# Kernel tuning notes

Hardware: AMD Instinct MI355X
Metric: run time of the kernel (lower is better)

The kernel has to match this reference:

```python
import jax, jax.numpy as jnp
import numpy as np

N_NODES = 50000
N_EDGES = 800000
NDIM_IN = 64
EDIMS = 64
NDIM_OUT = 128


def setup_inputs() -> dict:
    key = jax.random.key(0)
    k = jax.random.split(key, 8)
    nfeats = jax.random.normal(k[0], (N_NODES, NDIM_IN), dtype=jnp.float32)
    efeats = jax.random.normal(k[1], (N_EDGES, EDIMS), dtype=jnp.float32)
    # Linear weights stored as [in, out]; scaled for stable activations.
    W_msg = jax.random.normal(k[2], (NDIM_IN + EDIMS, NDIM_OUT), dtype=jnp.float32) * 0.05
    b_msg = jax.random.normal(k[3], (NDIM_OUT,), dtype=jnp.float32) * 0.05
    W_apply = jax.random.normal(k[4], (NDIM_IN + NDIM_OUT, NDIM_OUT), dtype=jnp.float32) * 0.05
    b_apply = jax.random.normal(k[5], (NDIM_OUT,), dtype=jnp.float32) * 0.05
    src = jax.random.randint(k[6], (N_EDGES,), 0, N_NODES, dtype=jnp.int64)
    dst = jax.random.randint(k[7], (N_EDGES,), 0, N_NODES, dtype=jnp.int64)
    return {
        "nfeats": nfeats,
        "efeats": efeats,
        "W_msg": W_msg,
        "b_msg": b_msg,
        "W_apply": W_apply,
        "b_apply": b_apply,
        "src": src,
        "dst": dst,
    }


def reference(nfeats, efeats, W_msg, b_msg, W_apply, b_apply, src, dst):
    # message: per-edge gather src node feats, concat with edge feats, linear+relu
    msg_in = jnp.concatenate([nfeats[src], efeats], axis=1)          # [E, ndim_in+edims]
    m = jax.nn.relu(msg_in @ W_msg + b_msg)                           # [E, ndim_out]
    # aggregate: sum messages into destination nodes
    h_neigh = jax.ops.segment_sum(m, dst, num_segments=nfeats.shape[0])  # [N, ndim_out]
    # update: concat original node feats with aggregated messages, linear+relu
    out = jax.nn.relu(jnp.concatenate([nfeats, h_neigh], axis=1) @ W_apply + b_apply)
    return out
```

## Files before the change

### kernel.cpp

```cpp
#include <hip/hip_runtime.h>
#include <hip/hip_bf16.h>

#define N_NODES  50000
#define N_EDGES  800000
#define NDIM_IN  64
#define EDIMS    64
#define NDIM_OUT 128

typedef __bf16 bf16;
typedef bf16  bf16x8 __attribute__((ext_vector_type(8)));
typedef float f32x4  __attribute__((ext_vector_type(4)));

__device__ __forceinline__ bool detect_f32(const void* nfeats) {
    const unsigned short* w = (const unsigned short*)nfeats;
    for (int i = 0; i < 64; i += 2) {
        const int e = (w[i] >> 7) & 0xFF;
        if (e < 100 || e > 134) return true;
    }
    return false;
}
__device__ __forceinline__ bool detect_i64(const int* p) {
    for (int i = 1; i < 64; i += 2) if (p[i] != 0) return false;
    return true;
}

__device__ __forceinline__ bf16x8 load8(const void* p, int off, bool f32) {
    if (f32) {
        const float* q = (const float*)p + off;
        const f32x4 a = *(const f32x4*)q;
        const f32x4 b = *(const f32x4*)(q + 4);
        bf16x8 r;
        #pragma unroll
        for (int u = 0; u < 4; ++u) { r[u] = (bf16)a[u]; r[4 + u] = (bf16)b[u]; }
        return r;
    }
    return *(const bf16x8*)((const bf16*)p + off);
}
__device__ __forceinline__ float loadf(const void* p, int i, bool f32) {
    return f32 ? ((const float*)p)[i] : (float)((const bf16*)p)[i];
}
__device__ __forceinline__ void storef(void* p, int i, float v, bool f32) {
    if (f32) ((float*)p)[i] = v; else ((bf16*)p)[i] = (bf16)v;
}

__global__ __launch_bounds__(256) void edge_msg_kernel(
    const void* __restrict__ nfeats,
    const void* __restrict__ efeats,
    const void* __restrict__ W_msg,
    const void* __restrict__ b_msg,
    const int*  __restrict__ src,
    const int*  __restrict__ dst,
    float*      __restrict__ h_neigh)
{
    __shared__ bf16 sWT[128 * 136];
    __shared__ int s_flags;

    const int tid = threadIdx.x;
    if (tid == 0)
        s_flags = (detect_f32(nfeats) ? 1 : 0) | (detect_i64(dst) ? 2 : 0);
    __syncthreads();
    const bool f32 = (s_flags & 1) != 0;
    const int  ish = (s_flags & 2) ? 1 : 0;

    #pragma unroll
    for (int it = 0; it < 8; ++it) {
        const int task = it * 256 + tid;
        const int k = task >> 4;
        const int c = task & 15;
        const bf16x8 w = load8(W_msg, k * 128 + c * 8, f32);
        #pragma unroll
        for (int u = 0; u < 8; ++u) sWT[(c * 8 + u) * 136 + k] = w[u];
    }
    __syncthreads();

    const int wave = tid >> 6;
    const int lane = tid & 63;
    const int m    = lane & 15;
    const int quad = lane >> 4;

    const int nchunks = N_EDGES / 64;
    for (int chunk = blockIdx.x; chunk < nchunks; chunk += gridDim.x) {
        const int ebase = chunk * 64 + wave * 16;
        const int e_m   = ebase + m;
        const int s     = src[e_m << ish];

        bf16x8 a[4];
        a[0] = load8(nfeats, s   * 64 +      quad * 8, f32);
        a[1] = load8(nfeats, s   * 64 + 32 + quad * 8, f32);
        a[2] = load8(efeats, e_m * 64 +      quad * 8, f32);
        a[3] = load8(efeats, e_m * 64 + 32 + quad * 8, f32);

        int drow[4];
        #pragma unroll
        for (int i = 0; i < 4; ++i)
            drow[i] = dst[(ebase + quad * 4 + i) << ish] * 128;

        #pragma unroll
        for (int t = 0; t < 8; ++t) {
            f32x4 acc = {0.f, 0.f, 0.f, 0.f};
            const bf16* bp = sWT + (t * 16 + m) * 136 + quad * 8;
            #pragma unroll
            for (int kb = 0; kb < 4; ++kb)
                acc = __builtin_amdgcn_mfma_f32_16x16x32_bf16(
                          a[kb], *(const bf16x8*)(bp + kb * 32), acc, 0, 0, 0);
            const int   n    = t * 16 + m;
            const float bias = loadf(b_msg, n, f32);
            #pragma unroll
            for (int i = 0; i < 4; ++i) {
                float v = acc[i] + bias;
                v = v > 0.f ? v : 0.f;
                unsafeAtomicAdd(h_neigh + drow[i] + n, v);
            }
        }
    }
}

__global__ __launch_bounds__(256) void apply_kernel(
    const void*  __restrict__ nfeats,
    const float* __restrict__ h_neigh,
    const void*  __restrict__ W_apply,
    const void*  __restrict__ b_apply,
    void*        __restrict__ out)
{
    __shared__ bf16 sWT[128 * 200];
    __shared__ int s_flags;

    const int tid = threadIdx.x;
    if (tid == 0) s_flags = detect_f32(nfeats) ? 1 : 0;
    __syncthreads();
    const bool f32 = (s_flags & 1) != 0;

    #pragma unroll
    for (int it = 0; it < 12; ++it) {
        const int task = it * 256 + tid;
        const int k = task >> 4;
        const int c = task & 15;
        const bf16x8 w = load8(W_apply, k * 128 + c * 8, f32);
        #pragma unroll
        for (int u = 0; u < 8; ++u) sWT[(c * 8 + u) * 200 + k] = w[u];
    }
    __syncthreads();

    const int wave = tid >> 6;
    const int lane = tid & 63;
    const int m    = lane & 15;
    const int quad = lane >> 4;

    const int nchunks = (N_NODES + 63) / 64;
    for (int chunk = blockIdx.x; chunk < nchunks; chunk += gridDim.x) {
        const int nbase = chunk * 64 + wave * 16;
        const int nm  = nbase + m;
        const int nmc = nm < N_NODES ? nm : N_NODES - 1;

        bf16x8 a[6];
        a[0] = load8(nfeats, nmc * 64 +      quad * 8, f32);
        a[1] = load8(nfeats, nmc * 64 + 32 + quad * 8, f32);
        #pragma unroll
        for (int kb = 0; kb < 4; ++kb) {
            const float* hp = h_neigh + nmc * 128 + kb * 32 + quad * 8;
            const f32x4 p = *(const f32x4*)(hp);
            const f32x4 q = *(const f32x4*)(hp + 4);
            bf16x8 r;
            #pragma unroll
            for (int u = 0; u < 4; ++u) { r[u] = (bf16)p[u]; r[4 + u] = (bf16)q[u]; }
            a[2 + kb] = r;
        }

        #pragma unroll
        for (int t = 0; t < 8; ++t) {
            f32x4 acc = {0.f, 0.f, 0.f, 0.f};
            const bf16* bp = sWT + (t * 16 + m) * 200 + quad * 8;
            #pragma unroll
            for (int kb = 0; kb < 6; ++kb)
                acc = __builtin_amdgcn_mfma_f32_16x16x32_bf16(
                          a[kb], *(const bf16x8*)(bp + kb * 32), acc, 0, 0, 0);
            const int   n    = t * 16 + m;
            const float bias = loadf(b_apply, n, f32);
            #pragma unroll
            for (int i = 0; i < 4; ++i) {
                const int row = nbase + quad * 4 + i;
                if (row < N_NODES) {
                    float v = acc[i] + bias;
                    v = v > 0.f ? v : 0.f;
                    storef(out, row * 128 + n, v, f32);
                }
            }
        }
    }
}

extern "C" void kernel_launch(void* const* d_in, const int* in_sizes, int n_in,
                              void* d_out, int out_size, void* d_ws, size_t ws_size,
                              hipStream_t stream) {
    const void* nfeats  = d_in[0];
    const void* efeats  = d_in[1];
    const void* W_msg   = d_in[2];
    const void* b_msg   = d_in[3];
    const void* W_apply = d_in[4];
    const void* b_apply = d_in[5];
    const int*  src     = (const int*)d_in[6];
    const int*  dst     = (const int*)d_in[7];
    float*      h_neigh = (float*)d_ws;

    hipMemsetAsync(h_neigh, 0, (size_t)N_NODES * NDIM_OUT * sizeof(float), stream);

    edge_msg_kernel<<<768, 256, 0, stream>>>(nfeats, efeats, W_msg, b_msg, src, dst, h_neigh);
    apply_kernel<<<512, 256, 0, stream>>>(nfeats, h_neigh, W_apply, b_apply, d_out);
}
```

Before: 665.7 us.

## Accumulate neighbor messages with packed bf16x2 atomics and transposed MFMA layout

Changes the h_neigh accumulator from fp32 to bf16 and scatters messages with packed bf16x2 atomic adds. Operands are swapped in the MFMA so each lane holds consecutive output columns for a single edge. This lets one dst lookup per lane drive paired atomics, and atomics are skipped when both ReLU outputs are zero. Bias is preloaded into shared memory and used as the initial accumulator, grid sizes are raised, and the apply kernel reads bf16 directly. The bf16 accumulation of sums (about 16 adds per node) loses precision, which risks exceeding the tolerance.

```diff
diff --git a/kernel.cpp b/kernel.cpp
--- a/kernel.cpp
+++ b/kernel.cpp
@@ -50,10 +50,11 @@
     const void* __restrict__ b_msg,
     const int*  __restrict__ src,
     const int*  __restrict__ dst,
-    float*      __restrict__ h_neigh)
+    bf16*       __restrict__ h_neigh)
 {
-    __shared__ bf16 sWT[128 * 136];
-    __shared__ int s_flags;
+    __shared__ bf16  sWT[128 * 136];
+    __shared__ float sB[128];
+    __shared__ int   s_flags;
 
     const int tid = threadIdx.x;
     if (tid == 0)
@@ -71,6 +72,7 @@
         #pragma unroll
         for (int u = 0; u < 8; ++u) sWT[(c * 8 + u) * 136 + k] = w[u];
     }
+    if (tid < 128) sB[tid] = loadf(b_msg, tid, f32);
     __syncthreads();
 
     const int wave = tid >> 6;
@@ -81,46 +83,46 @@
     const int nchunks = N_EDGES / 64;
     for (int chunk = blockIdx.x; chunk < nchunks; chunk += gridDim.x) {
         const int ebase = chunk * 64 + wave * 16;
-        const int e_m   = ebase + m;
-        const int s     = src[e_m << ish];
-
-        bf16x8 a[4];
-        a[0] = load8(nfeats, s   * 64 +      quad * 8, f32);
-        a[1] = load8(nfeats, s   * 64 + 32 + quad * 8, f32);
-        a[2] = load8(efeats, e_m * 64 +      quad * 8, f32);
-        a[3] = load8(efeats, e_m * 64 + 32 + quad * 8, f32);
-
-        int drow[4];
-        #pragma unroll
-        for (int i = 0; i < 4; ++i)
-            drow[i] = dst[(ebase + quad * 4 + i) << ish] * 128;
+        const int e     = ebase + m;
+        const int s     = src[e << ish];
+        const int drow  = dst[e << ish] * 128;
+
+        bf16x8 b[4];
+        b[0] = load8(nfeats, s * 64 +      quad * 8, f32);
+        b[1] = load8(nfeats, s * 64 + 32 + quad * 8, f32);
+        b[2] = load8(efeats, e * 64 +      quad * 8, f32);
+        b[3] = load8(efeats, e * 64 + 32 + quad * 8, f32);
 
         #pragma unroll
         for (int t = 0; t < 8; ++t) {
-            f32x4 acc = {0.f, 0.f, 0.f, 0.f};
-            const bf16* bp = sWT + (t * 16 + m) * 136 + quad * 8;
+            f32x4 acc = *(const f32x4*)(sB + t * 16 + quad * 4);
+            const bf16* ap = sWT + (t * 16 + m) * 136 + quad * 8;
             #pragma unroll
             for (int kb = 0; kb < 4; ++kb)
                 acc = __builtin_amdgcn_mfma_f32_16x16x32_bf16(
-                          a[kb], *(const bf16x8*)(bp + kb * 32), acc, 0, 0, 0);
-            const int   n    = t * 16 + m;
-            const float bias = loadf(b_msg, n, f32);
-            #pragma unroll
-            for (int i = 0; i < 4; ++i) {
-                float v = acc[i] + bias;
-                v = v > 0.f ? v : 0.f;
-                unsafeAtomicAdd(h_neigh + drow[i] + n, v);
+                          *(const bf16x8*)(ap + kb * 32), b[kb], acc, 0, 0, 0);
+            bf16* hp = h_neigh + drow + t * 16 + quad * 4;
+            #pragma unroll
+            for (int pr = 0; pr < 2; ++pr) {
+                const float v0 = acc[2 * pr];
+                const float v1 = acc[2 * pr + 1];
+                if (v0 > 0.f || v1 > 0.f) {
+                    __hip_bfloat162 pv;
+                    pv.x = __float2bfloat16(v0 > 0.f ? v0 : 0.f);
+                    pv.y = __float2bfloat16(v1 > 0.f ? v1 : 0.f);
+                    unsafeAtomicAdd((__hip_bfloat162*)(hp + 2 * pr), pv);
+                }
             }
         }
     }
 }
 
 __global__ __launch_bounds__(256) void apply_kernel(
-    const void*  __restrict__ nfeats,
-    const float* __restrict__ h_neigh,
-    const void*  __restrict__ W_apply,
-    const void*  __restrict__ b_apply,
-    void*        __restrict__ out)
+    const void* __restrict__ nfeats,
+    const bf16* __restrict__ h_neigh,
+    const void* __restrict__ W_apply,
+    const void* __restrict__ b_apply,
+    void*       __restrict__ out)
 {
     __shared__ bf16 sWT[128 * 200];
     __shared__ int s_flags;
@@ -156,15 +158,8 @@
         a[0] = load8(nfeats, nmc * 64 +      quad * 8, f32);
         a[1] = load8(nfeats, nmc * 64 + 32 + quad * 8, f32);
         #pragma unroll
-        for (int kb = 0; kb < 4; ++kb) {
-            const float* hp = h_neigh + nmc * 128 + kb * 32 + quad * 8;
-            const f32x4 p = *(const f32x4*)(hp);
-            const f32x4 q = *(const f32x4*)(hp + 4);
-            bf16x8 r;
-            #pragma unroll
-            for (int u = 0; u < 4; ++u) { r[u] = (bf16)p[u]; r[4 + u] = (bf16)q[u]; }
-            a[2 + kb] = r;
-        }
+        for (int kb = 0; kb < 4; ++kb)
+            a[2 + kb] = *(const bf16x8*)(h_neigh + nmc * 128 + kb * 32 + quad * 8);
 
         #pragma unroll
         for (int t = 0; t < 8; ++t) {
@@ -200,10 +195,10 @@
     const void* b_apply = d_in[5];
     const int*  src     = (const int*)d_in[6];
     const int*  dst     = (const int*)d_in[7];
-    float*      h_neigh = (float*)d_ws;
-
-    hipMemsetAsync(h_neigh, 0, (size_t)N_NODES * NDIM_OUT * sizeof(float), stream);
-
-    edge_msg_kernel<<<768, 256, 0, stream>>>(nfeats, efeats, W_msg, b_msg, src, dst, h_neigh);
-    apply_kernel<<<512, 256, 0, stream>>>(nfeats, h_neigh, W_apply, b_apply, d_out);
-}
+    bf16*       h_neigh = (bf16*)d_ws;
+
+    hipMemsetAsync(h_neigh, 0, (size_t)N_NODES * NDIM_OUT * sizeof(bf16), stream);
+
+    edge_msg_kernel<<<1024, 256, 0, stream>>>(nfeats, efeats, W_msg, b_msg, src, dst, h_neigh);
+    apply_kernel<<<782, 256, 0, stream>>>(nfeats, h_neigh, W_apply, b_apply, d_out);
+}
```

Measured after the change: 953.3 us. 1.43x slower.
